# Performance work log

Measured on AMD Instinct MI355X. Metric: run time of the kernel, lower is better.

The kernel has to match this reference:

```python
import jax, jax.numpy as jnp
import numpy as np

B, S, D = 2, 2048, 768
NH, GH = 12, 4
HD = D // NH            # 64
GD = HD * GH            # 256 (grouped KV projection width)
REP = NH // GH          # 3  (repeat factor for KV heads)
SCALE = HD ** -0.5
MASK_FILL = -1e-09      # faithful to the original (NOT -1e9)


def setup_inputs() -> dict:
    key = jax.random.key(0)
    ks = jax.random.split(key, 9)
    init = 0.02
    x = jax.random.normal(ks[0], (B, S, D), dtype=jnp.float32)
    masks = jnp.tril(jnp.ones((S, S), dtype=jnp.float32)) > 0  # bool causal mask
    Wq = jax.random.normal(ks[1], (D, D), dtype=jnp.float32) * init
    bq = jnp.zeros((D,), dtype=jnp.float32)
    Wk = jax.random.normal(ks[2], (D, GD), dtype=jnp.float32) * init
    bk = jnp.zeros((GD,), dtype=jnp.float32)
    Wv = jax.random.normal(ks[3], (D, GD), dtype=jnp.float32) * init
    bv = jnp.zeros((GD,), dtype=jnp.float32)
    Wo = jax.random.normal(ks[4], (D, D), dtype=jnp.float32) * init
    bo = jnp.zeros((D,), dtype=jnp.float32)
    return {"x": x, "masks": masks, "Wq": Wq, "bq": bq, "Wk": Wk, "bk": bk,
            "Wv": Wv, "bv": bv, "Wo": Wo, "bo": bo}


def reference(x, masks, Wq, bq, Wk, bk, Wv, bv, Wo, bo):
    bs, seq, _ = x.shape
    # projections (weights stored [in, out])
    q = (x @ Wq + bq).reshape(bs, seq, NH, HD).transpose(0, 2, 1, 3)   # [b, nh, s, hd]
    k = (x @ Wk + bk).reshape(bs, seq, GH, HD).transpose(0, 2, 1, 3)   # [b, gh, s, hd]
    v = (x @ Wv + bv).reshape(bs, seq, GH, HD).transpose(0, 2, 1, 3)
    # repeat_interleave KV heads to match query heads (faithful to original)
    k = jnp.repeat(k, REP, axis=1)                                     # [b, nh, s, hd]
    v = jnp.repeat(v, REP, axis=1)
    scores = jnp.einsum('bhqd,bhkd->bhqk', q, k) * SCALE               # [b, nh, s, s]
    # original: masked_fill(masks == 0, -1e-09)
    scores = jnp.where(masks, scores, MASK_FILL)
    attn = jax.nn.softmax(scores, axis=-1)
    out = jnp.einsum('bhqk,bhkd->bhqd', attn, v)                       # [b, nh, s, hd]
    # faithful to original buggy merge: transpose(-1,-2).contiguous().view(b, s, dim)
    out = out.transpose(0, 1, 3, 2).reshape(bs, seq, D)
    return out @ Wo + bo
```

## Files before the change

### kernel.cpp

```cpp
#include <hip/hip_runtime.h>
#include <stdint.h>


typedef unsigned short ushort_t;
typedef short bf16x8 __attribute__((ext_vector_type(8)));
typedef float f32x4 __attribute__((ext_vector_type(4)));

#define MFMA(a, b, c) __builtin_amdgcn_mfma_f32_16x16x32_bf16((a), (b), (c), 0, 0, 0)

__device__ __forceinline__ ushort_t f2bf(float f) {
    union { float f; unsigned u; } v; v.f = f;
    const unsigned r = v.u + 0x7FFFu + ((v.u >> 16) & 1u);
    return (ushort_t)(r >> 16);
}

__global__ __launch_bounds__(256) void prep_x(const float* __restrict__ x,
                                              ushort_t* __restrict__ xb) {
    const int i = (blockIdx.x * 256 + threadIdx.x) * 4;
    const float4 v = *(const float4*)(x + i);
    uint2 p;
    p.x = (unsigned)f2bf(v.x) | ((unsigned)f2bf(v.y) << 16);
    p.y = (unsigned)f2bf(v.z) | ((unsigned)f2bf(v.w) << 16);
    *(uint2*)(xb + i) = p;
}

__global__ __launch_bounds__(256) void prep_w(
    const float* __restrict__ Wq, const float* __restrict__ Wk,
    const float* __restrict__ Wv, const float* __restrict__ Wo,
    ushort_t* __restrict__ WqT, ushort_t* __restrict__ WkT,
    ushort_t* __restrict__ WvT, ushort_t* __restrict__ WoT) {
    const int z = blockIdx.z;
    const float* src; ushort_t* dst; int N;
    if (z == 0)      { src = Wq; dst = WqT; N = 768; }
    else if (z == 1) { src = Wk; dst = WkT; N = 256; }
    else if (z == 2) { src = Wv; dst = WvT; N = 256; }
    else             { src = Wo; dst = WoT; N = 768; }
    const int k0 = blockIdx.x * 64, n0 = blockIdx.y * 64;
    if (n0 >= N) return;

    __shared__ float Ts[64][65];
    const int tid = threadIdx.x;
    const int r = tid >> 2, cb = (tid & 3) * 16;
    #pragma unroll
    for (int jj = 0; jj < 4; ++jj) {
        const float4 v = *(const float4*)(src + (k0 + r) * N + n0 + cb + jj * 4);
        Ts[cb + jj * 4 + 0][r] = v.x; Ts[cb + jj * 4 + 1][r] = v.y;
        Ts[cb + jj * 4 + 2][r] = v.z; Ts[cb + jj * 4 + 3][r] = v.w;
    }
    __syncthreads();
    const int n = tid >> 2, kc = (tid & 3) * 16;
    unsigned hbuf[16];
    #pragma unroll
    for (int j = 0; j < 16; ++j) hbuf[j] = f2bf(Ts[n][kc + j]);
    uint4 p0, p1;
    p0.x = hbuf[0] | (hbuf[1] << 16);   p0.y = hbuf[2] | (hbuf[3] << 16);
    p0.z = hbuf[4] | (hbuf[5] << 16);   p0.w = hbuf[6] | (hbuf[7] << 16);
    p1.x = hbuf[8] | (hbuf[9] << 16);   p1.y = hbuf[10] | (hbuf[11] << 16);
    p1.z = hbuf[12] | (hbuf[13] << 16); p1.w = hbuf[14] | (hbuf[15] << 16);
    *(uint4*)(dst + (n0 + n) * 768 + k0 + kc) = p0;
    *(uint4*)(dst + (n0 + n) * 768 + k0 + kc + 8) = p1;
}

__global__ __launch_bounds__(256) void qkv_kernel(
    const ushort_t* __restrict__ xb,
    const ushort_t* __restrict__ WqT, const ushort_t* __restrict__ WkT,
    const ushort_t* __restrict__ WvT,
    const float* __restrict__ bq, const float* __restrict__ bk,
    const float* __restrict__ bv,
    ushort_t* __restrict__ Qb, ushort_t* __restrict__ Kb,
    ushort_t* __restrict__ Vtb) {
    const int ct = blockIdx.x, rt = blockIdx.y;
    const int r0 = rt * 64;
    const ushort_t* WT; const float* bias; int head; int kind;
    if (ct < 12)      { WT = WqT; bias = bq; head = ct;      kind = 0; }
    else if (ct < 16) { WT = WkT; bias = bk; head = ct - 12; kind = 1; }
    else              { WT = WvT; bias = bv; head = ct - 16; kind = 2; }
    const int n0 = head * 64;

    __shared__ uint4 Xs[512];
    __shared__ uint4 Ws[512];

    const int tid = threadIdx.x;
    const int lane = tid & 63, w = tid >> 6;
    const int quad = lane >> 4, l15 = lane & 15;
    const int sr = tid >> 2, sb = (tid & 3) * 2;

    f32x4 acc[4] = {{0,0,0,0},{0,0,0,0},{0,0,0,0},{0,0,0,0}};

    for (int k0 = 0; k0 < 768; k0 += 64) {
        __syncthreads();
        #pragma unroll
        for (int c = 0; c < 2; ++c) {
            const int blk = sb + c;
            Xs[sr * 8 + (blk ^ (sr & 7))] = *(const uint4*)(xb + (r0 + sr) * 768 + k0 + blk * 8);
            Ws[sr * 8 + (blk ^ (sr & 7))] = *(const uint4*)(WT + (n0 + sr) * 768 + k0 + blk * 8);
        }
        __syncthreads();
        #pragma unroll
        for (int ks = 0; ks < 2; ++ks) {
            const int arow = 16 * w + l15;
            const bf16x8 af = *(const bf16x8*)&Xs[arow * 8 + ((quad + 4 * ks) ^ (arow & 7))];
            #pragma unroll
            for (int ctt = 0; ctt < 4; ++ctt) {
                const int brow = 16 * ctt + l15;
                const bf16x8 bfr = *(const bf16x8*)&Ws[brow * 8 + ((quad + 4 * ks) ^ (brow & 7))];
                acc[ctt] = MFMA(af, bfr, acc[ctt]);
            }
        }
    }
    #pragma unroll
    for (int ctt = 0; ctt < 4; ++ctt) {
        const int cd = ctt * 16 + l15;
        const float bv_ = bias[n0 + cd];
        const int row0 = r0 + 16 * w + quad * 4;
        const int b = row0 >> 11;
        if (kind == 2) {
            const int s0 = row0 & 2047;
            unsigned h[4];
            #pragma unroll
            for (int reg = 0; reg < 4; ++reg) h[reg] = f2bf(acc[ctt][reg] + bv_);
            uint2 pk; pk.x = h[0] | (h[1] << 16); pk.y = h[2] | (h[3] << 16);
            *(uint2*)(Vtb + ((b * 4 + head) * 64 + cd) * 2048 + s0) = pk;
        } else {
            #pragma unroll
            for (int reg = 0; reg < 4; ++reg) {
                const int row = row0 + reg;
                const int s = row & 2047;
                const ushort_t h = f2bf(acc[ctt][reg] + bv_);
                if (kind == 0) Qb[((b * 12 + head) * 2048 + s) * 64 + cd] = h;
                else           Kb[((b * 4 + head) * 2048 + s) * 64 + cd] = h;
            }
        }
    }
}

__global__ __launch_bounds__(256) void attn_kernel(
    const ushort_t* __restrict__ Qb, const ushort_t* __restrict__ Kb,
    const ushort_t* __restrict__ Vtb,
    ushort_t* __restrict__ aT_hi, ushort_t* __restrict__ aT_lo) {
    const int qt = blockIdx.x, h = blockIdx.y, b = blockIdx.z;
    const int g = h / 3;
    const int q0 = qt * 64;
    const int tid = threadIdx.x;
    const int lane = tid & 63, w = tid >> 6;
    const int quad = lane >> 4, l15 = lane & 15;

    __shared__ uint4 K_l[512];
    __shared__ uint4 V_l[512];
    __shared__ __align__(16) ushort_t P_l[64 * 72];

    const ushort_t* Qp = Qb + ((b * 12 + h) * 2048 + q0 + 16 * w + l15) * 64;
    const bf16x8 qf0 = *(const bf16x8*)(Qp + quad * 8);
    const bf16x8 qf1 = *(const bf16x8*)(Qp + 32 + quad * 8);

    const ushort_t* Kp = Kb + (b * 4 + g) * 2048 * 64;
    const ushort_t* Vp = Vtb + (b * 4 + g) * 64 * 2048;

    f32x4 o[4] = {{0,0,0,0},{0,0,0,0},{0,0,0,0},{0,0,0,0}};
    float lacc[4] = {0.f, 0.f, 0.f, 0.f};

    const int sr = tid >> 2, sb = (tid & 3) * 2;
    const int qg = q0 + 16 * w + quad * 4;

    for (int k0 = 0; k0 < 2048; k0 += 64) {
        __syncthreads();
        #pragma unroll
        for (int c = 0; c < 2; ++c) {
            const int blk = sb + c;
            K_l[sr * 8 + (blk ^ (sr & 7))] = *(const uint4*)(Kp + (k0 + sr) * 64 + blk * 8);
            V_l[sr * 8 + (blk ^ (sr & 7))] = *(const uint4*)(Vp + sr * 2048 + k0 + blk * 8);
        }
        __syncthreads();
        #pragma unroll
        for (int ctt = 0; ctt < 4; ++ctt) {
            const int key = ctt * 16 + l15;
            f32x4 s = {0, 0, 0, 0};
            s = MFMA(qf0, *(const bf16x8*)&K_l[key * 8 + ((quad + 0) ^ (key & 7))], s);
            s = MFMA(qf1, *(const bf16x8*)&K_l[key * 8 + ((quad + 4) ^ (key & 7))], s);
            const int kg = k0 + key;
            #pragma unroll
            for (int reg = 0; reg < 4; ++reg) {
                const float sv = (kg <= qg + reg) ? s[reg] * 0.125f : -1e-9f;
                const float e = __expf(sv);
                lacc[reg] += e;
                P_l[(16 * w + quad * 4 + reg) * 72 + key] = f2bf(e);
            }
        }
        const bf16x8 pf0 = *(const bf16x8*)&P_l[(16 * w + l15) * 72 + quad * 8];
        const bf16x8 pf1 = *(const bf16x8*)&P_l[(16 * w + l15) * 72 + 32 + quad * 8];
        #pragma unroll
        for (int ctt = 0; ctt < 4; ++ctt) {
            const int d = ctt * 16 + l15;
            o[ctt] = MFMA(pf0, *(const bf16x8*)&V_l[d * 8 + ((quad + 0) ^ (d & 7))], o[ctt]);
            o[ctt] = MFMA(pf1, *(const bf16x8*)&V_l[d * 8 + ((quad + 4) ^ (d & 7))], o[ctt]);
        }
    }
    #pragma unroll
    for (int reg = 0; reg < 4; ++reg) {
        float v = lacc[reg];
        v += __shfl_xor(v, 1); v += __shfl_xor(v, 2);
        v += __shfl_xor(v, 4); v += __shfl_xor(v, 8);
        lacc[reg] = 1.f / v;
    }
    const int t0 = q0 + 16 * w + quad * 4;
    #pragma unroll
    for (int ctt = 0; ctt < 4; ++ctt) {
        const int d = ctt * 16 + l15;
        unsigned hh[4], hl[4];
        #pragma unroll
        for (int reg = 0; reg < 4; ++reg) {
            const float val = o[ctt][reg] * lacc[reg];
            const ushort_t hi = f2bf(val);
            union { unsigned u; float f; } vv; vv.u = (unsigned)hi << 16;
            hh[reg] = hi;
            hl[reg] = f2bf(val - vv.f);
        }
        const int idx = (b * 768 + h * 64 + d) * 2048 + t0;
        uint2 ph, pl;
        ph.x = hh[0] | (hh[1] << 16); ph.y = hh[2] | (hh[3] << 16);
        pl.x = hl[0] | (hl[1] << 16); pl.y = hl[2] | (hl[3] << 16);
        *(uint2*)(aT_hi + idx) = ph;
        *(uint2*)(aT_lo + idx) = pl;
    }
}

__global__ __launch_bounds__(256) void out_proj_kernel(
    const ushort_t* __restrict__ aT_hi, const ushort_t* __restrict__ aT_lo,
    const ushort_t* __restrict__ WoT, const float* __restrict__ bo,
    float* __restrict__ out) {
    const int ct = blockIdx.x, rt = blockIdx.y;
    const int r0 = rt * 64, c0 = ct * 64;
    __shared__ uint4 Ah[512];
    __shared__ uint4 Al[512];
    __shared__ uint4 Ws[512];
    const int tid = threadIdx.x;
    const int lane = tid & 63, w = tid >> 6;
    const int quad = lane >> 4, l15 = lane & 15;
    const int sr = tid >> 2, sb = (tid & 3) * 2;

    f32x4 acc[4] = {{0,0,0,0},{0,0,0,0},{0,0,0,0},{0,0,0,0}};

    for (int k0 = 0; k0 < 768; k0 += 64) {
        __syncthreads();
        #pragma unroll
        for (int c = 0; c < 2; ++c) {
            const int blk = sb + c;
            const int slot = sr * 8 + (blk ^ (sr & 7));
            Ah[slot] = *(const uint4*)(aT_hi + (r0 + sr) * 768 + k0 + blk * 8);
            Al[slot] = *(const uint4*)(aT_lo + (r0 + sr) * 768 + k0 + blk * 8);
            Ws[slot] = *(const uint4*)(WoT + (c0 + sr) * 768 + k0 + blk * 8);
        }
        __syncthreads();
        #pragma unroll
        for (int ks = 0; ks < 2; ++ks) {
            const int arow = 16 * w + l15;
            const int aslot = arow * 8 + ((quad + 4 * ks) ^ (arow & 7));
            const bf16x8 ah = *(const bf16x8*)&Ah[aslot];
            const bf16x8 al = *(const bf16x8*)&Al[aslot];
            #pragma unroll
            for (int ctt = 0; ctt < 4; ++ctt) {
                const int brow = 16 * ctt + l15;
                const bf16x8 bfr = *(const bf16x8*)&Ws[brow * 8 + ((quad + 4 * ks) ^ (brow & 7))];
                acc[ctt] = MFMA(ah, bfr, acc[ctt]);
                acc[ctt] = MFMA(al, bfr, acc[ctt]);
            }
        }
    }
    #pragma unroll
    for (int ctt = 0; ctt < 4; ++ctt) {
        const int cd = c0 + ctt * 16 + l15;
        const float bo_v = bo[cd];
        #pragma unroll
        for (int reg = 0; reg < 4; ++reg) {
            const int row = r0 + 16 * w + quad * 4 + reg;
            out[row * 768 + cd] = acc[ctt][reg] + bo_v;
        }
    }
}

extern "C" void kernel_launch(void* const* d_in, const int* in_sizes, int n_in,
                              void* d_out, int out_size, void* d_ws, size_t ws_size,
                              hipStream_t stream) {
    const float* x  = (const float*)d_in[0];
    const float* Wq = (const float*)d_in[2];
    const float* bq = (const float*)d_in[3];
    const float* Wk = (const float*)d_in[4];
    const float* bk = (const float*)d_in[5];
    const float* Wv = (const float*)d_in[6];
    const float* bv = (const float*)d_in[7];
    const float* Wo = (const float*)d_in[8];
    const float* bo = (const float*)d_in[9];
    float* out = (float*)d_out;

    uint8_t* wsb = (uint8_t*)d_ws;
    ushort_t* xb    = (ushort_t*)(wsb);
    ushort_t* WqT   = (ushort_t*)(wsb + 6291456);
    ushort_t* WkT   = (ushort_t*)(wsb + 7471104);
    ushort_t* WvT   = (ushort_t*)(wsb + 7864320);
    ushort_t* WoT   = (ushort_t*)(wsb + 8257536);
    ushort_t* Qb    = (ushort_t*)(wsb + 9437184);
    ushort_t* Kb    = (ushort_t*)(wsb + 15728640);
    ushort_t* Vtb   = (ushort_t*)(wsb + 17825792);
    ushort_t* aT_hi = (ushort_t*)(wsb + 19922944);
    ushort_t* aT_lo = (ushort_t*)(wsb + 26214400);

    prep_x<<<3072, 256, 0, stream>>>(x, xb);
    prep_w<<<dim3(12, 12, 4), 256, 0, stream>>>(Wq, Wk, Wv, Wo, WqT, WkT, WvT, WoT);
    qkv_kernel<<<dim3(20, 64), 256, 0, stream>>>(xb, WqT, WkT, WvT, bq, bk, bv, Qb, Kb, Vtb);
    attn_kernel<<<dim3(32, 12, 2), 256, 0, stream>>>(Qb, Kb, Vtb, aT_hi, aT_lo);
    out_proj_kernel<<<dim3(12, 64), 256, 0, stream>>>(aT_hi, aT_lo, WoT, bo, out);
}
```

Baseline: 201.9 us.

## Replace masked attention tail with V suffix sums and skip masked key tiles

```diff
diff --git a/kernel.cpp b/kernel.cpp
--- a/kernel.cpp
+++ b/kernel.cpp
@@ -126,19 +126,51 @@
             for (int reg = 0; reg < 4; ++reg) {
                 const int row = row0 + reg;
                 const int s = row & 2047;
-                const ushort_t h = f2bf(acc[ctt][reg] + bv_);
-                if (kind == 0) Qb[((b * 12 + head) * 2048 + s) * 64 + cd] = h;
-                else           Kb[((b * 4 + head) * 2048 + s) * 64 + cd] = h;
-            }
+                const float pre = acc[ctt][reg] + bv_;
+                const ushort_t hh = f2bf((kind == 0) ? pre * 0.125f : pre);
+                if (kind == 0) Qb[((b * 12 + head) * 2048 + s) * 64 + cd] = hh;
+                else           Kb[((b * 4 + head) * 2048 + s) * 64 + cd] = hh;
+            }
+        }
+    }
+}
+
+__global__ __launch_bounds__(256) void v_suffix_kernel(
+    const ushort_t* __restrict__ Vtb, float* __restrict__ SV) {
+    const int b = blockIdx.z, g = blockIdx.y, d0 = blockIdx.x * 8;
+    const int tid = threadIdx.x;
+    const int dd = tid >> 5, tt = tid & 31;
+    const ushort_t* vp = Vtb + ((b * 4 + g) * 64 + d0 + dd) * 2048 + tt * 64;
+    float s = 0.f;
+    #pragma unroll
+    for (int j = 0; j < 8; ++j) {
+        const bf16x8 v = *(const bf16x8*)(vp + j * 8);
+        #pragma unroll
+        for (int e = 0; e < 8; ++e) {
+            union { unsigned u; float f; } c;
+            c.u = ((unsigned)(ushort_t)v[e]) << 16;
+            s += c.f;
+        }
+    }
+    __shared__ float cs[8][32];
+    cs[dd][tt] = s;
+    __syncthreads();
+    if (tid < 8) {
+        float run = 0.f;
+        const int base = ((b * 4 + g) * 32) * 64 + d0 + tid;
+        for (int j = 31; j >= 0; --j) {
+            run += cs[tid][j];
+            SV[base + j * 64] = run;
         }
     }
 }
 
 __global__ __launch_bounds__(256) void attn_kernel(
     const ushort_t* __restrict__ Qb, const ushort_t* __restrict__ Kb,
-    const ushort_t* __restrict__ Vtb,
+    const ushort_t* __restrict__ Vtb, const float* __restrict__ SV,
     ushort_t* __restrict__ aT_hi, ushort_t* __restrict__ aT_lo) {
-    const int qt = blockIdx.x, h = blockIdx.y, b = blockIdx.z;
+    const int qt = 31 - (int)blockIdx.x;
+    const int h = blockIdx.y, b = blockIdx.z;
     const int g = h / 3;
     const int q0 = qt * 64;
     const int tid = threadIdx.x;
@@ -161,15 +193,30 @@
 
     const int sr = tid >> 2, sb = (tid & 3) * 2;
     const int qg = q0 + 16 * w + quad * 4;
-
-    for (int k0 = 0; k0 < 2048; k0 += 64) {
-        __syncthreads();
+    const int prow = (16 * w + quad * 4) * 72;
+
+    auto stage_kv = [&](int k0) {
         #pragma unroll
         for (int c = 0; c < 2; ++c) {
             const int blk = sb + c;
             K_l[sr * 8 + (blk ^ (sr & 7))] = *(const uint4*)(Kp + (k0 + sr) * 64 + blk * 8);
             V_l[sr * 8 + (blk ^ (sr & 7))] = *(const uint4*)(Vp + sr * 2048 + k0 + blk * 8);
         }
+    };
+    auto do_pv = [&]() {
+        const bf16x8 pf0 = *(const bf16x8*)&P_l[(16 * w + l15) * 72 + quad * 8];
+        const bf16x8 pf1 = *(const bf16x8*)&P_l[(16 * w + l15) * 72 + 32 + quad * 8];
+        #pragma unroll
+        for (int ctt = 0; ctt < 4; ++ctt) {
+            const int d = ctt * 16 + l15;
+            o[ctt] = MFMA(pf0, *(const bf16x8*)&V_l[d * 8 + ((quad + 0) ^ (d & 7))], o[ctt]);
+            o[ctt] = MFMA(pf1, *(const bf16x8*)&V_l[d * 8 + ((quad + 4) ^ (d & 7))], o[ctt]);
+        }
+    };
+
+    for (int k0 = 0; k0 < q0; k0 += 64) {
+        __syncthreads();
+        stage_kv(k0);
         __syncthreads();
         #pragma unroll
         for (int ctt = 0; ctt < 4; ++ctt) {
@@ -177,30 +224,55 @@
             f32x4 s = {0, 0, 0, 0};
             s = MFMA(qf0, *(const bf16x8*)&K_l[key * 8 + ((quad + 0) ^ (key & 7))], s);
             s = MFMA(qf1, *(const bf16x8*)&K_l[key * 8 + ((quad + 4) ^ (key & 7))], s);
-            const int kg = k0 + key;
             #pragma unroll
             for (int reg = 0; reg < 4; ++reg) {
-                const float sv = (kg <= qg + reg) ? s[reg] * 0.125f : -1e-9f;
-                const float e = __expf(sv);
+                const float e = __expf(s[reg]);
                 lacc[reg] += e;
-                P_l[(16 * w + quad * 4 + reg) * 72 + key] = f2bf(e);
-            }
-        }
-        const bf16x8 pf0 = *(const bf16x8*)&P_l[(16 * w + l15) * 72 + quad * 8];
-        const bf16x8 pf1 = *(const bf16x8*)&P_l[(16 * w + l15) * 72 + 32 + quad * 8];
+                P_l[prow + reg * 72 + key] = f2bf(e);
+            }
+        }
+        do_pv();
+    }
+
+    {
+        __syncthreads();
+        stage_kv(q0);
+        __syncthreads();
         #pragma unroll
         for (int ctt = 0; ctt < 4; ++ctt) {
-            const int d = ctt * 16 + l15;
-            o[ctt] = MFMA(pf0, *(const bf16x8*)&V_l[d * 8 + ((quad + 0) ^ (d & 7))], o[ctt]);
-            o[ctt] = MFMA(pf1, *(const bf16x8*)&V_l[d * 8 + ((quad + 4) ^ (d & 7))], o[ctt]);
-        }
-    }
+            const int key = ctt * 16 + l15;
+            f32x4 s = {0, 0, 0, 0};
+            s = MFMA(qf0, *(const bf16x8*)&K_l[key * 8 + ((quad + 0) ^ (key & 7))], s);
+            s = MFMA(qf1, *(const bf16x8*)&K_l[key * 8 + ((quad + 4) ^ (key & 7))], s);
+            const int kg = q0 + key;
+            #pragma unroll
+            for (int reg = 0; reg < 4; ++reg) {
+                float e = __expf(s[reg]);
+                e = (kg <= qg + reg) ? e : 1.0f;
+                lacc[reg] += e;
+                P_l[prow + reg * 72 + key] = f2bf(e);
+            }
+        }
+        do_pv();
+    }
+
+    if (qt < 31) {
+        const float* svp = SV + ((b * 4 + g) * 32 + qt + 1) * 64;
+        #pragma unroll
+        for (int ctt = 0; ctt < 4; ++ctt) {
+            const float t = svp[ctt * 16 + l15];
+            #pragma unroll
+            for (int reg = 0; reg < 4; ++reg) o[ctt][reg] += t;
+        }
+    }
+    const float tailc = (float)(2048 - 64 - q0);
+
     #pragma unroll
     for (int reg = 0; reg < 4; ++reg) {
         float v = lacc[reg];
         v += __shfl_xor(v, 1); v += __shfl_xor(v, 2);
         v += __shfl_xor(v, 4); v += __shfl_xor(v, 8);
-        lacc[reg] = 1.f / v;
+        lacc[reg] = 1.f / (v + tailc);
     }
     const int t0 = q0 + 16 * w + quad * 4;
     #pragma unroll
@@ -303,10 +375,12 @@
     ushort_t* Vtb   = (ushort_t*)(wsb + 17825792);
     ushort_t* aT_hi = (ushort_t*)(wsb + 19922944);
     ushort_t* aT_lo = (ushort_t*)(wsb + 26214400);
+    float* SV = (float*)wsb;
 
     prep_x<<<3072, 256, 0, stream>>>(x, xb);
     prep_w<<<dim3(12, 12, 4), 256, 0, stream>>>(Wq, Wk, Wv, Wo, WqT, WkT, WvT, WoT);
     qkv_kernel<<<dim3(20, 64), 256, 0, stream>>>(xb, WqT, WkT, WvT, bq, bk, bv, Qb, Kb, Vtb);
-    attn_kernel<<<dim3(32, 12, 2), 256, 0, stream>>>(Qb, Kb, Vtb, aT_hi, aT_lo);
+    v_suffix_kernel<<<dim3(8, 4, 2), 256, 0, stream>>>(Vtb, SV);
+    attn_kernel<<<dim3(32, 12, 2), 256, 0, stream>>>(Qb, Kb, Vtb, SV, aT_hi, aT_lo);
     out_proj_kernel<<<dim3(12, 64), 256, 0, stream>>>(aT_hi, aT_lo, WoT, bo, out);
 }
```

New measurement: 200.7 us. No clear change (-0.6%).
